# Optimization experiments

Measured on AMD Instinct MI355X. Metric: run time of the kernel, lower is better.

The kernel has to match this reference:

```python
import jax, jax.numpy as jnp
import numpy as np

S, B, I, H = 2048, 4096, 2, 6  # seq, batch, input_size, hidden_size


def setup_inputs() -> dict:
    key = jax.random.key(0)
    ks = jax.random.split(key, 11)
    init = lambda k, sh: jax.random.normal(k, sh, dtype=jnp.float32) * 0.1
    return {
        "x": jax.random.normal(ks[0], (S, B, I), dtype=jnp.float32),
        # layer-0 LSTM params (PyTorch gate order: i, f, g, o)
        "Wih0": init(ks[1], (4 * H, I)),
        "Whh0": init(ks[2], (4 * H, H)),
        "bih0": init(ks[3], (4 * H,)),
        "bhh0": init(ks[4], (4 * H,)),
        # layer-1 LSTM params
        "Wih1": init(ks[5], (4 * H, H)),
        "Whh1": init(ks[6], (4 * H, H)),
        "bih1": init(ks[7], (4 * H,)),
        "bhh1": init(ks[8], (4 * H,)),
        # final Linear(6, 1)
        "W2": init(ks[9], (1, H)),
        "b2": init(ks[10], (1,)),
    }


def _lstm_layer(x, Wih, Whh, bih, bhh):
    # x: (S, B, in_dim) -> hidden outputs (S, B, H)
    Bn = x.shape[1]
    Hn = Whh.shape[1]
    b = bih + bhh
    # precompute input projections for all timesteps at once (memory-bound GEMM)
    xg = jnp.einsum("sbi,gi->sbg", x, Wih) + b  # (S, B, 4H)

    def step(carry, xt_g):
        h, c = carry
        g = xt_g + h @ Whh.T  # (B, 4H)
        i, f, gg, o = jnp.split(g, 4, axis=-1)
        i = jax.nn.sigmoid(i)
        f = jax.nn.sigmoid(f)
        gg = jnp.tanh(gg)
        o = jax.nn.sigmoid(o)
        c = f * c + i * gg
        h = o * jnp.tanh(c)
        return (h, c), h

    h0 = jnp.zeros((Bn, Hn), dtype=x.dtype)
    c0 = jnp.zeros((Bn, Hn), dtype=x.dtype)
    _, hs = jax.lax.scan(step, (h0, c0), xg)
    return hs  # (S, B, H)


def reference(x, Wih0, Whh0, bih0, bhh0, Wih1, Whh1, bih1, bhh1, W2, b2):
    h1 = _lstm_layer(x, Wih0, Whh0, bih0, bhh0)   # (S, B, H)
    h2 = _lstm_layer(h1, Wih1, Whh1, bih1, bhh1)  # (S, B, H); dropout disabled (eval)
    flat = h2.reshape(-1, H)                       # (S*B, H)
    out = flat @ W2.T + b2                         # (S*B, 1) — original discards final view
    return out
```

## Files before the change

### kernel.cpp

```cpp
#include <hip/hip_runtime.h>

#define SEQ   2048
#define BATCH 4096
#define HID   6
#define BLK   256

typedef float v2f __attribute__((ext_vector_type(2)));
typedef unsigned u2 __attribute__((ext_vector_type(2)));

__device__ __forceinline__ float fexp2(float a) {
#if __has_builtin(__builtin_amdgcn_exp2f)
  return __builtin_amdgcn_exp2f(a);
#else
  float r; asm("v_exp_f32 %0, %1" : "=v"(r) : "v"(a)); return r;
#endif
}
__device__ __forceinline__ float frcp(float a) {
#if __has_builtin(__builtin_amdgcn_rcpf)
  return __builtin_amdgcn_rcpf(a);
#else
  float r; asm("v_rcp_f32 %0, %1" : "=v"(r) : "v"(a)); return r;
#endif
}

template <int OFF>
__device__ __forceinline__ float swzf(float v) {
  int r = __builtin_amdgcn_ds_swizzle(__builtin_bit_cast(int, v), OFF);
  return __builtin_bit_cast(float, r);
}
#define BC0 0x18
#define BC1 0x38
#define BC2 0x58
#define BC3 0x78
#define BC4 0x98
#define BC5 0xB8

__device__ __forceinline__ float xhalf(float v, bool hi) {
#if __has_builtin(__builtin_amdgcn_permlane32_swap)
  u2 r = __builtin_amdgcn_permlane32_swap(__builtin_bit_cast(unsigned, v),
                                          __builtin_bit_cast(unsigned, v), false, false);
  return __builtin_bit_cast(float, hi ? r.x : r.y);
#else
  unsigned d = __builtin_bit_cast(unsigned, v), s = d;
  asm volatile("v_permlane32_swap_b32 %0, %1" : "+v"(d), "+v"(s));
  return __builtin_bit_cast(float, hi ? d : s);
#endif
}

__global__ __launch_bounds__(BLK, 1) void lstm2_kernel(
    const float* __restrict__ x,
    const float* __restrict__ Wih0, const float* __restrict__ Whh0,
    const float* __restrict__ bih0, const float* __restrict__ bhh0,
    const float* __restrict__ Wih1, const float* __restrict__ Whh1,
    const float* __restrict__ bih1, const float* __restrict__ bhh1,
    const float* __restrict__ W2,   const float* __restrict__ b2,
    float* __restrict__ out)
{
  __shared__ float obuf[64][16];

  const int tid = threadIdx.x;
  const int wib = tid >> 6;
  const int l6  = tid & 63;
  const bool hi = l6 >= 32;
  const int j   = l6 & 31;
  const int el  = j >> 3;
  const int u   = j & 7;
  const int uu  = (u < HID) ? u : (HID - 1);
  const int b   = blockIdx.x * 16 + wib * 4 + el;

  v2f WA[4][3], WB[4][3];
  float BS[4];
#pragma unroll
  for (int q = 0; q < 4; ++q) {
    const int rq = q * HID + uu;
    const float Kq = (q == 2) ? -2.8853900817779268f : -1.4426950408889634f;
    if (!hi) {
      WA[q][0] = v2f{Kq * Wih0[rq * 2 + 0], Kq * Wih0[rq * 2 + 1]};
      WA[q][1] = v2f{0.f, 0.f};
      WA[q][2] = v2f{0.f, 0.f};
#pragma unroll
      for (int k = 0; k < 3; ++k)
        WB[q][k] = v2f{Kq * Whh0[rq * HID + 2 * k], Kq * Whh0[rq * HID + 2 * k + 1]};
      BS[q] = Kq * (bih0[rq] + bhh0[rq]);
    } else {
#pragma unroll
      for (int k = 0; k < 3; ++k) {
        WA[q][k] = v2f{Kq * Wih1[rq * HID + 2 * k], Kq * Wih1[rq * HID + 2 * k + 1]};
        WB[q][k] = v2f{Kq * Whh1[rq * HID + 2 * k], Kq * Whh1[rq * HID + 2 * k + 1]};
      }
      BS[q] = Kq * (bih1[rq] + bhh1[rq]);
    }
  }
  const v2f w2p0 = v2f{W2[0], W2[1]}, w2p1 = v2f{W2[2], W2[3]}, w2p2 = v2f{W2[4], W2[5]};
  const float bout = b2[0];
  const float KT = 2.8853900817779268f;

  float h = 0.f, c = 0.f;

  auto gath = [&](float hv, v2f (&g)[3]) {
    g[0] = v2f{swzf<BC0>(hv), swzf<BC1>(hv)};
    g[1] = v2f{swzf<BC2>(hv), swzf<BC3>(hv)};
    g[2] = v2f{swzf<BC4>(hv), swzf<BC5>(hv)};
  };

  auto step = [&](v2f xc, float& ov) {
    v2f g2[3]; gath(h, g2);
    float hs = xhalf(h, hi);
    v2f g1[3]; gath(hs, g1);
    v2f v10 = hi ? g1[0] : xc;

    float a[4];
#pragma unroll
    for (int q = 0; q < 4; ++q) {
      v2f acc = v2f{BS[q], 0.f};
      acc = __builtin_elementwise_fma(WA[q][0], v10,   acc);
      acc = __builtin_elementwise_fma(WA[q][1], g1[1], acc);
      acc = __builtin_elementwise_fma(WA[q][2], g1[2], acc);
      acc = __builtin_elementwise_fma(WB[q][0], g2[0], acc);
      acc = __builtin_elementwise_fma(WB[q][1], g2[1], acc);
      acc = __builtin_elementwise_fma(WB[q][2], g2[2], acc);
      a[q] = acc.x + acc.y;
    }
    v2f ao = __builtin_elementwise_fma(w2p0, g2[0],
             __builtin_elementwise_fma(w2p1, g2[1],
             __builtin_elementwise_fma(w2p2, g2[2], v2f{bout, 0.f})));
    ov = ao.x + ao.y;

    float i_ = frcp(1.f + fexp2(a[0]));
    float f_ = frcp(1.f + fexp2(a[1]));
    float g_ = fmaf(2.f, frcp(1.f + fexp2(a[2])), -1.f);
    float o_ = frcp(1.f + fexp2(a[3]));
    c = fmaf(f_, c, i_ * g_);
    float th = fmaf(-2.f, frcp(1.f + fexp2(c * KT)), 1.f);
    h = o_ * th;
  };

  auto flush = [&](int rbase) {
    const int r = tid >> 2, jj = (tid & 3) * 4;
    float4 vv = *(const float4*)&obuf[r][jj];
    *(float4*)&out[(size_t)(rbase + r) * BATCH + blockIdx.x * 16 + jj] = vv;
  };

  const v2f* x2 = (const v2f*)x;
  v2f xc  = x2[(size_t)0 * BATCH + b];
  v2f xn1 = x2[(size_t)1 * BATCH + b];
  v2f xn2 = x2[(size_t)2 * BATCH + b];
  v2f xn3 = x2[(size_t)3 * BATCH + b];

  {
    float ov;
    step(xc, ov);
    if (hi) { h = 0.f; c = 0.f; }
    v2f xf = x2[(size_t)4 * BATCH + b];
    xc = xn1; xn1 = xn2; xn2 = xn3; xn3 = xf;
  }

#pragma unroll 1
  for (int t = 1; t < SEQ; ++t) {
    int tf = t + 4; tf = (tf < SEQ) ? tf : (SEQ - 1);
    v2f xf = x2[(size_t)tf * BATCH + b];

    float ov;
    step(xc, ov);

    if (t >= 2) {
      const int r = t - 2;
      if (hi && u == 0) obuf[r & 63][wib * 4 + el] = ov;
      if ((r & 63) == 63) {
        __syncthreads();
        flush(r - 63);
        __syncthreads();
      }
    }
    xc = xn1; xn1 = xn2; xn2 = xn3; xn3 = xf;
  }

  {
    float ov;
    step(xc, ov);
    if (hi && u == 0) obuf[62][wib * 4 + el] = ov;
    v2f g2[3]; gath(h, g2);
    v2f ao = __builtin_elementwise_fma(w2p0, g2[0],
             __builtin_elementwise_fma(w2p1, g2[1],
             __builtin_elementwise_fma(w2p2, g2[2], v2f{bout, 0.f})));
    if (hi && u == 0) obuf[63][wib * 4 + el] = ao.x + ao.y;
    __syncthreads();
    flush(SEQ - 64);
  }
}

extern "C" void kernel_launch(void* const* d_in, const int* in_sizes, int n_in,
                              void* d_out, int out_size, void* d_ws, size_t ws_size,
                              hipStream_t stream) {
  const float* x    = (const float*)d_in[0];
  const float* Wih0 = (const float*)d_in[1];
  const float* Whh0 = (const float*)d_in[2];
  const float* bih0 = (const float*)d_in[3];
  const float* bhh0 = (const float*)d_in[4];
  const float* Wih1 = (const float*)d_in[5];
  const float* Whh1 = (const float*)d_in[6];
  const float* bih1 = (const float*)d_in[7];
  const float* bhh1 = (const float*)d_in[8];
  const float* W2   = (const float*)d_in[9];
  const float* b2   = (const float*)d_in[10];
  float* out = (float*)d_out;

  dim3 grid(BATCH / 16);
  dim3 block(BLK);
  hipLaunchKernelGGL(lstm2_kernel, grid, block, 0, stream,
                     x, Wih0, Whh0, bih0, bhh0, Wih1, Whh1, bih1, bhh1, W2, b2, out);
}
```

Measured before the change: 621.0 us.

## Replace ds_swizzle broadcasts with DPP xor-permutation gather and permuted weights

Swaps the six ds_swizzle broadcasts per gather for DPP quad and row permutations (xor patterns). Each lane then receives hidden values in a lane-dependent order, so the weight matrices are pre-permuted per lane by u^k with zero padding for the lanes beyond HID. The aim is to drop the LDS-path swizzle latency from the serial recurrence and keep cross-lane movement in VALU DPP. The cost is an extra v2f FMA per gate and split accumulators to shorten the dependency chain.

```diff
diff --git a/kernel.cpp b/kernel.cpp
--- a/kernel.cpp
+++ b/kernel.cpp
@@ -23,17 +23,11 @@
 #endif
 }
 
-template <int OFF>
-__device__ __forceinline__ float swzf(float v) {
-  int r = __builtin_amdgcn_ds_swizzle(__builtin_bit_cast(int, v), OFF);
+template <int CTRL>
+__device__ __forceinline__ float dppf(float v) {
+  int r = __builtin_amdgcn_update_dpp(0, __builtin_bit_cast(int, v), CTRL, 0xF, 0xF, true);
   return __builtin_bit_cast(float, r);
 }
-#define BC0 0x18
-#define BC1 0x38
-#define BC2 0x58
-#define BC3 0x78
-#define BC4 0x98
-#define BC5 0xB8
 
 __device__ __forceinline__ float xhalf(float v, bool hi) {
 #if __has_builtin(__builtin_amdgcn_permlane32_swap)
@@ -68,62 +62,78 @@
   const int uu  = (u < HID) ? u : (HID - 1);
   const int b   = blockIdx.x * 16 + wib * 4 + el;
 
-  v2f WA[4][3], WB[4][3];
+  v2f WA[4][4], WB[4][4], w2r[4];
   float BS[4];
 #pragma unroll
   for (int q = 0; q < 4; ++q) {
     const int rq = q * HID + uu;
     const float Kq = (q == 2) ? -2.8853900817779268f : -1.4426950408889634f;
-    if (!hi) {
-      WA[q][0] = v2f{Kq * Wih0[rq * 2 + 0], Kq * Wih0[rq * 2 + 1]};
-      WA[q][1] = v2f{0.f, 0.f};
-      WA[q][2] = v2f{0.f, 0.f};
-#pragma unroll
-      for (int k = 0; k < 3; ++k)
-        WB[q][k] = v2f{Kq * Whh0[rq * HID + 2 * k], Kq * Whh0[rq * HID + 2 * k + 1]};
-      BS[q] = Kq * (bih0[rq] + bhh0[rq]);
-    } else {
-#pragma unroll
-      for (int k = 0; k < 3; ++k) {
-        WA[q][k] = v2f{Kq * Wih1[rq * HID + 2 * k], Kq * Wih1[rq * HID + 2 * k + 1]};
-        WB[q][k] = v2f{Kq * Whh1[rq * HID + 2 * k], Kq * Whh1[rq * HID + 2 * k + 1]};
+#pragma unroll
+    for (int k = 0; k < 4; ++k) {
+      const int k0 = u ^ (2 * k), k1 = u ^ (2 * k + 1);
+      const bool ok0 = (k0 < HID), ok1 = (k1 < HID);
+      if (!hi) {
+        WA[q][k] = v2f{0.f, 0.f};
+        WB[q][k] = v2f{ok0 ? Kq * Whh0[rq * HID + k0] : 0.f,
+                       ok1 ? Kq * Whh0[rq * HID + k1] : 0.f};
+      } else {
+        WA[q][k] = v2f{ok0 ? Kq * Wih1[rq * HID + k0] : 0.f,
+                       ok1 ? Kq * Wih1[rq * HID + k1] : 0.f};
+        WB[q][k] = v2f{ok0 ? Kq * Whh1[rq * HID + k0] : 0.f,
+                       ok1 ? Kq * Whh1[rq * HID + k1] : 0.f};
       }
-      BS[q] = Kq * (bih1[rq] + bhh1[rq]);
     }
-  }
-  const v2f w2p0 = v2f{W2[0], W2[1]}, w2p1 = v2f{W2[2], W2[3]}, w2p2 = v2f{W2[4], W2[5]};
+    if (!hi) WA[q][0] = v2f{Kq * Wih0[rq * 2 + 0], Kq * Wih0[rq * 2 + 1]};
+    BS[q] = Kq * ((!hi ? bih0[rq] : bih1[rq]) + (!hi ? bhh0[rq] : bhh1[rq]));
+  }
+#pragma unroll
+  for (int k = 0; k < 4; ++k) {
+    const int k0 = u ^ (2 * k), k1 = u ^ (2 * k + 1);
+    w2r[k] = v2f{(k0 < HID) ? W2[k0] : 0.f, (k1 < HID) ? W2[k1] : 0.f};
+  }
   const float bout = b2[0];
   const float KT = 2.8853900817779268f;
 
   float h = 0.f, c = 0.f;
 
-  auto gath = [&](float hv, v2f (&g)[3]) {
-    g[0] = v2f{swzf<BC0>(hv), swzf<BC1>(hv)};
-    g[1] = v2f{swzf<BC2>(hv), swzf<BC3>(hv)};
-    g[2] = v2f{swzf<BC4>(hv), swzf<BC5>(hv)};
+  auto gath = [&](float hv, v2f (&g)[4]) {
+    float t1 = dppf<0xB1>(hv);
+    float t2 = dppf<0x4E>(hv);
+    float t3 = dppf<0x4E>(t1);
+    float m  = dppf<0x141>(hv);
+    float m1 = dppf<0xB1>(m);
+    float m2 = dppf<0x4E>(m);
+    float m3 = dppf<0x4E>(m1);
+    g[0] = v2f{hv, t1};
+    g[1] = v2f{t2, t3};
+    g[2] = v2f{m3, m2};
+    g[3] = v2f{m1, m};
   };
 
   auto step = [&](v2f xc, float& ov) {
-    v2f g2[3]; gath(h, g2);
+    v2f g2[4]; gath(h, g2);
     float hs = xhalf(h, hi);
-    v2f g1[3]; gath(hs, g1);
+    v2f g1[4]; gath(hs, g1);
     v2f v10 = hi ? g1[0] : xc;
 
     float a[4];
 #pragma unroll
     for (int q = 0; q < 4; ++q) {
-      v2f acc = v2f{BS[q], 0.f};
-      acc = __builtin_elementwise_fma(WA[q][0], v10,   acc);
-      acc = __builtin_elementwise_fma(WA[q][1], g1[1], acc);
-      acc = __builtin_elementwise_fma(WA[q][2], g1[2], acc);
-      acc = __builtin_elementwise_fma(WB[q][0], g2[0], acc);
-      acc = __builtin_elementwise_fma(WB[q][1], g2[1], acc);
-      acc = __builtin_elementwise_fma(WB[q][2], g2[2], acc);
+      v2f accA = __builtin_elementwise_fma(WA[q][0], v10, v2f{BS[q], 0.f});
+      accA = __builtin_elementwise_fma(WA[q][1], g1[1], accA);
+      accA = __builtin_elementwise_fma(WA[q][2], g1[2], accA);
+      accA = __builtin_elementwise_fma(WA[q][3], g1[3], accA);
+      v2f accB = WB[q][0] * g2[0];
+      accB = __builtin_elementwise_fma(WB[q][1], g2[1], accB);
+      accB = __builtin_elementwise_fma(WB[q][2], g2[2], accB);
+      accB = __builtin_elementwise_fma(WB[q][3], g2[3], accB);
+      v2f acc = accA + accB;
       a[q] = acc.x + acc.y;
     }
-    v2f ao = __builtin_elementwise_fma(w2p0, g2[0],
-             __builtin_elementwise_fma(w2p1, g2[1],
-             __builtin_elementwise_fma(w2p2, g2[2], v2f{bout, 0.f})));
+    v2f ao = __builtin_elementwise_fma(w2r[0], g2[0],
+             __builtin_elementwise_fma(w2r[1], g2[1],
+             __builtin_elementwise_fma(w2r[2], g2[2],
+             __builtin_elementwise_fma(w2r[3], g2[3], v2f{bout, 0.f}))));
     ov = ao.x + ao.y;
 
     float i_ = frcp(1.f + fexp2(a[0]));
@@ -179,10 +189,11 @@
     float ov;
     step(xc, ov);
     if (hi && u == 0) obuf[62][wib * 4 + el] = ov;
-    v2f g2[3]; gath(h, g2);
-    v2f ao = __builtin_elementwise_fma(w2p0, g2[0],
-             __builtin_elementwise_fma(w2p1, g2[1],
-             __builtin_elementwise_fma(w2p2, g2[2], v2f{bout, 0.f})));
+    v2f g2[4]; gath(h, g2);
+    v2f ao = __builtin_elementwise_fma(w2r[0], g2[0],
+             __builtin_elementwise_fma(w2r[1], g2[1],
+             __builtin_elementwise_fma(w2r[2], g2[2],
+             __builtin_elementwise_fma(w2r[3], g2[3], v2f{bout, 0.f}))));
     if (hi && u == 0) obuf[63][wib * 4 + el] = ao.x + ao.y;
     __syncthreads();
     flush(SEQ - 64);
```

New measurement: 651.4 us. 4.9% more time.

## Split LSTM gate computation across lane pairs to double parallelism per batch element

Applied to the files above, without the earlier changes.

Each batch element now uses 32 lanes instead of 16, so each lane computes only two of the four gates, and the partner gates are exchanged with a DPP row shift. The grid doubles to 8 batch elements per block, and launch bounds allow two blocks per CU. The intent is to shorten the serial per-timestep dependency chain (fewer FMAs and transcendentals per lane) and raise occupancy. The cost is twice as many lanes doing the gather swizzles and an extra cross-lane exchange each step.

```diff
diff --git a/kernel.cpp b/kernel.cpp
--- a/kernel.cpp
+++ b/kernel.cpp
@@ -23,6 +23,12 @@
 #endif
 }
 
+template <int CTRL>
+__device__ __forceinline__ float dppf(float v) {
+  int r = __builtin_amdgcn_update_dpp(0, __builtin_bit_cast(int, v), CTRL, 0xF, 0xF, true);
+  return __builtin_bit_cast(float, r);
+}
+
 template <int OFF>
 __device__ __forceinline__ float swzf(float v) {
   int r = __builtin_amdgcn_ds_swizzle(__builtin_bit_cast(int, v), OFF);
@@ -35,19 +41,19 @@
 #define BC4 0x98
 #define BC5 0xB8
 
-__device__ __forceinline__ float xhalf(float v, bool hi) {
-#if __has_builtin(__builtin_amdgcn_permlane32_swap)
-  u2 r = __builtin_amdgcn_permlane32_swap(__builtin_bit_cast(unsigned, v),
+__device__ __forceinline__ float xor16f(float v, bool hi) {
+#if __has_builtin(__builtin_amdgcn_permlane16_swap)
+  u2 r = __builtin_amdgcn_permlane16_swap(__builtin_bit_cast(unsigned, v),
                                           __builtin_bit_cast(unsigned, v), false, false);
   return __builtin_bit_cast(float, hi ? r.x : r.y);
 #else
   unsigned d = __builtin_bit_cast(unsigned, v), s = d;
-  asm volatile("v_permlane32_swap_b32 %0, %1" : "+v"(d), "+v"(s));
+  asm volatile("v_permlane16_swap_b32 %0, %1" : "+v"(d), "+v"(s));
   return __builtin_bit_cast(float, hi ? d : s);
 #endif
 }
 
-__global__ __launch_bounds__(BLK, 1) void lstm2_kernel(
+__global__ __launch_bounds__(BLK, 2) void lstm2_kernel(
     const float* __restrict__ x,
     const float* __restrict__ Wih0, const float* __restrict__ Whh0,
     const float* __restrict__ bih0, const float* __restrict__ bhh0,
@@ -56,44 +62,54 @@
     const float* __restrict__ W2,   const float* __restrict__ b2,
     float* __restrict__ out)
 {
-  __shared__ float obuf[64][16];
+  __shared__ float obuf[64][8];
 
   const int tid = threadIdx.x;
   const int wib = tid >> 6;
   const int l6  = tid & 63;
-  const bool hi = l6 >= 32;
-  const int j   = l6 & 31;
-  const int el  = j >> 3;
-  const int u   = j & 7;
+  const int el  = l6 >> 5;
+  const int r5  = l6 & 31;
+  const bool hiL = (r5 & 16) != 0;
+  const int p   = (r5 >> 3) & 1;
+  const int u   = r5 & 7;
   const int uu  = (u < HID) ? u : (HID - 1);
-  const int b   = blockIdx.x * 16 + wib * 4 + el;
-
-  v2f WA[4][3], WB[4][3];
-  float BS[4];
+  const int b   = blockIdx.x * 8 + wib * 2 + el;
+
+  const int r0 = p ? (2 * HID + uu) : uu;
+  const int r1 = p ? (3 * HID + uu) : (HID + uu);
+  const float A  = p ? 2.f : 1.f;
+  const float Bc = p ? -1.f : 0.f;
+  const float K0 = p ? -2.8853900817779268f : -1.4426950408889634f;
+  const float K1 = -1.4426950408889634f;
+  const float KT =  2.8853900817779268f;
+
+  v2f WA0[3], WA1[3], WB0[3], WB1[3];
+  float BS0, BS1;
+  if (!hiL) {
+    WA0[0] = v2f{K0 * Wih0[r0 * 2 + 0], K0 * Wih0[r0 * 2 + 1]};
+    WA1[0] = v2f{K1 * Wih0[r1 * 2 + 0], K1 * Wih0[r1 * 2 + 1]};
+    WA0[1] = v2f{0.f, 0.f}; WA0[2] = v2f{0.f, 0.f};
+    WA1[1] = v2f{0.f, 0.f}; WA1[2] = v2f{0.f, 0.f};
 #pragma unroll
-  for (int q = 0; q < 4; ++q) {
-    const int rq = q * HID + uu;
-    const float Kq = (q == 2) ? -2.8853900817779268f : -1.4426950408889634f;
-    if (!hi) {
-      WA[q][0] = v2f{Kq * Wih0[rq * 2 + 0], Kq * Wih0[rq * 2 + 1]};
-      WA[q][1] = v2f{0.f, 0.f};
-      WA[q][2] = v2f{0.f, 0.f};
+    for (int k = 0; k < 3; ++k) {
+      WB0[k] = v2f{K0 * Whh0[r0 * HID + 2 * k], K0 * Whh0[r0 * HID + 2 * k + 1]};
+      WB1[k] = v2f{K1 * Whh0[r1 * HID + 2 * k], K1 * Whh0[r1 * HID + 2 * k + 1]};
+    }
+    BS0 = K0 * (bih0[r0] + bhh0[r0]);
+    BS1 = K1 * (bih0[r1] + bhh0[r1]);
+  } else {
 #pragma unroll
-      for (int k = 0; k < 3; ++k)
-        WB[q][k] = v2f{Kq * Whh0[rq * HID + 2 * k], Kq * Whh0[rq * HID + 2 * k + 1]};
-      BS[q] = Kq * (bih0[rq] + bhh0[rq]);
-    } else {
-#pragma unroll
-      for (int k = 0; k < 3; ++k) {
-        WA[q][k] = v2f{Kq * Wih1[rq * HID + 2 * k], Kq * Wih1[rq * HID + 2 * k + 1]};
-        WB[q][k] = v2f{Kq * Whh1[rq * HID + 2 * k], Kq * Whh1[rq * HID + 2 * k + 1]};
-      }
-      BS[q] = Kq * (bih1[rq] + bhh1[rq]);
+    for (int k = 0; k < 3; ++k) {
+      WA0[k] = v2f{K0 * Wih1[r0 * HID + 2 * k], K0 * Wih1[r0 * HID + 2 * k + 1]};
+      WA1[k] = v2f{K1 * Wih1[r1 * HID + 2 * k], K1 * Wih1[r1 * HID + 2 * k + 1]};
+      WB0[k] = v2f{K0 * Whh1[r0 * HID + 2 * k], K0 * Whh1[r0 * HID + 2 * k + 1]};
+      WB1[k] = v2f{K1 * Whh1[r1 * HID + 2 * k], K1 * Whh1[r1 * HID + 2 * k + 1]};
     }
+    BS0 = K0 * (bih1[r0] + bhh1[r0]);
+    BS1 = K1 * (bih1[r1] + bhh1[r1]);
   }
   const v2f w2p0 = v2f{W2[0], W2[1]}, w2p1 = v2f{W2[2], W2[3]}, w2p2 = v2f{W2[4], W2[5]};
   const float bout = b2[0];
-  const float KT = 2.8853900817779268f;
 
   float h = 0.f, c = 0.f;
 
@@ -105,40 +121,47 @@
 
   auto step = [&](v2f xc, float& ov) {
     v2f g2[3]; gath(h, g2);
-    float hs = xhalf(h, hi);
+    float hs = xor16f(h, hiL);
     v2f g1[3]; gath(hs, g1);
-    v2f v10 = hi ? g1[0] : xc;
-
-    float a[4];
-#pragma unroll
-    for (int q = 0; q < 4; ++q) {
-      v2f acc = v2f{BS[q], 0.f};
-      acc = __builtin_elementwise_fma(WA[q][0], v10,   acc);
-      acc = __builtin_elementwise_fma(WA[q][1], g1[1], acc);
-      acc = __builtin_elementwise_fma(WA[q][2], g1[2], acc);
-      acc = __builtin_elementwise_fma(WB[q][0], g2[0], acc);
-      acc = __builtin_elementwise_fma(WB[q][1], g2[1], acc);
-      acc = __builtin_elementwise_fma(WB[q][2], g2[2], acc);
-      a[q] = acc.x + acc.y;
-    }
+    v2f v10 = hiL ? g1[0] : xc;
+
+    v2f a0v = __builtin_elementwise_fma(WA0[0], v10, v2f{BS0, 0.f});
+    a0v = __builtin_elementwise_fma(WA0[1], g1[1], a0v);
+    a0v = __builtin_elementwise_fma(WA0[2], g1[2], a0v);
+    a0v = __builtin_elementwise_fma(WB0[0], g2[0], a0v);
+    a0v = __builtin_elementwise_fma(WB0[1], g2[1], a0v);
+    a0v = __builtin_elementwise_fma(WB0[2], g2[2], a0v);
+    float a0 = a0v.x + a0v.y;
+
+    v2f a1v = __builtin_elementwise_fma(WA1[0], v10, v2f{BS1, 0.f});
+    a1v = __builtin_elementwise_fma(WA1[1], g1[1], a1v);
+    a1v = __builtin_elementwise_fma(WA1[2], g1[2], a1v);
+    a1v = __builtin_elementwise_fma(WB1[0], g2[0], a1v);
+    a1v = __builtin_elementwise_fma(WB1[1], g2[1], a1v);
+    a1v = __builtin_elementwise_fma(WB1[2], g2[2], a1v);
+    float a1 = a1v.x + a1v.y;
+
     v2f ao = __builtin_elementwise_fma(w2p0, g2[0],
              __builtin_elementwise_fma(w2p1, g2[1],
              __builtin_elementwise_fma(w2p2, g2[2], v2f{bout, 0.f})));
     ov = ao.x + ao.y;
 
-    float i_ = frcp(1.f + fexp2(a[0]));
-    float f_ = frcp(1.f + fexp2(a[1]));
-    float g_ = fmaf(2.f, frcp(1.f + fexp2(a[2])), -1.f);
-    float o_ = frcp(1.f + fexp2(a[3]));
-    c = fmaf(f_, c, i_ * g_);
+    float g0  = fmaf(A, frcp(1.f + fexp2(a0)), Bc);
+    float g1v = frcp(1.f + fexp2(a1));
+    float xg0 = dppf<0x128>(g0);
+    float xg1 = dppf<0x128>(g1v);
+    float m = g0 * xg0;
+    float f = p ? xg1 : g1v;
+    float o = p ? g1v : xg1;
+    c = fmaf(f, c, m);
     float th = fmaf(-2.f, frcp(1.f + fexp2(c * KT)), 1.f);
-    h = o_ * th;
+    h = o * th;
   };
 
   auto flush = [&](int rbase) {
-    const int r = tid >> 2, jj = (tid & 3) * 4;
-    float4 vv = *(const float4*)&obuf[r][jj];
-    *(float4*)&out[(size_t)(rbase + r) * BATCH + blockIdx.x * 16 + jj] = vv;
+    const int r = tid >> 2, jj = (tid & 3) * 2;
+    float2 vv = *(const float2*)&obuf[r][jj];
+    *(float2*)&out[(size_t)(rbase + r) * BATCH + blockIdx.x * 8 + jj] = vv;
   };
 
   const v2f* x2 = (const v2f*)x;
@@ -150,7 +173,7 @@
   {
     float ov;
     step(xc, ov);
-    if (hi) { h = 0.f; c = 0.f; }
+    if (hiL) { h = 0.f; c = 0.f; }
     v2f xf = x2[(size_t)4 * BATCH + b];
     xc = xn1; xn1 = xn2; xn2 = xn3; xn3 = xf;
   }
@@ -165,7 +188,7 @@
 
     if (t >= 2) {
       const int r = t - 2;
-      if (hi && u == 0) obuf[r & 63][wib * 4 + el] = ov;
+      if (hiL && p == 0 && u == 0) obuf[r & 63][wib * 2 + el] = ov;
       if ((r & 63) == 63) {
         __syncthreads();
         flush(r - 63);
@@ -178,12 +201,12 @@
   {
     float ov;
     step(xc, ov);
-    if (hi && u == 0) obuf[62][wib * 4 + el] = ov;
+    if (hiL && p == 0 && u == 0) obuf[62][wib * 2 + el] = ov;
     v2f g2[3]; gath(h, g2);
     v2f ao = __builtin_elementwise_fma(w2p0, g2[0],
              __builtin_elementwise_fma(w2p1, g2[1],
              __builtin_elementwise_fma(w2p2, g2[2], v2f{bout, 0.f})));
-    if (hi && u == 0) obuf[63][wib * 4 + el] = ao.x + ao.y;
+    if (hiL && p == 0 && u == 0) obuf[63][wib * 2 + el] = ao.x + ao.y;
     __syncthreads();
     flush(SEQ - 64);
   }
@@ -205,7 +228,7 @@
   const float* b2   = (const float*)d_in[10];
   float* out = (float*)d_out;
 
-  dim3 grid(BATCH / 16);
+  dim3 grid(BATCH / 8);
   dim3 block(BLK);
   hipLaunchKernelGGL(lstm2_kernel, grid, block, 0, stream,
                      x, Wih0, Whh0, bih0, bhh0, Wih1, Whh1, bih1, bhh1, W2, b2, out);
```

Measured after the change: 669.0 us. +7.7%, slower.

## Stage x in double-buffered LDS chunks and shorten the recurrent dependency chain

Applied to the files above, without the earlier changes.

Replaces the per-step global loads of x (software-pipelined four steps ahead) with coalesced 64-timestep chunk loads into a double-buffered shared-memory tile, refilled during the existing flush barriers. The gather path now runs permlane32_swap on the already-swizzled values instead of swizzling the swapped h again, and each gate dot product is split into two independent FMA chains. The aim is to cut global-load latency and length from the serial per-step critical path. In exchange it adds 16 KB of LDS, per-step LDS reads, and six permlane swaps in place of one swap plus six swizzles.

```diff
diff --git a/kernel.cpp b/kernel.cpp
--- a/kernel.cpp
+++ b/kernel.cpp
@@ -57,6 +57,7 @@
     float* __restrict__ out)
 {
   __shared__ float obuf[64][16];
+  __shared__ float xbuf[2][64][32];
 
   const int tid = threadIdx.x;
   const int wib = tid >> 6;
@@ -66,7 +67,8 @@
   const int el  = j >> 3;
   const int u   = j & 7;
   const int uu  = (u < HID) ? u : (HID - 1);
-  const int b   = blockIdx.x * 16 + wib * 4 + el;
+  const int elb = wib * 4 + el;
+  const int b   = blockIdx.x * 16 + elb;
 
   v2f WA[4][3], WB[4][3];
   float BS[4];
@@ -105,20 +107,22 @@
 
   auto step = [&](v2f xc, float& ov) {
     v2f g2[3]; gath(h, g2);
-    float hs = xhalf(h, hi);
-    v2f g1[3]; gath(hs, g1);
+    v2f g1[3];
+    g1[0] = v2f{xhalf(g2[0].x, hi), xhalf(g2[0].y, hi)};
+    g1[1] = v2f{xhalf(g2[1].x, hi), xhalf(g2[1].y, hi)};
+    g1[2] = v2f{xhalf(g2[2].x, hi), xhalf(g2[2].y, hi)};
     v2f v10 = hi ? g1[0] : xc;
 
     float a[4];
 #pragma unroll
     for (int q = 0; q < 4; ++q) {
-      v2f acc = v2f{BS[q], 0.f};
-      acc = __builtin_elementwise_fma(WA[q][0], v10,   acc);
-      acc = __builtin_elementwise_fma(WA[q][1], g1[1], acc);
-      acc = __builtin_elementwise_fma(WA[q][2], g1[2], acc);
-      acc = __builtin_elementwise_fma(WB[q][0], g2[0], acc);
-      acc = __builtin_elementwise_fma(WB[q][1], g2[1], acc);
-      acc = __builtin_elementwise_fma(WB[q][2], g2[2], acc);
+      v2f accA = __builtin_elementwise_fma(WA[q][0], v10, v2f{BS[q], 0.f});
+      accA = __builtin_elementwise_fma(WA[q][1], g1[1], accA);
+      accA = __builtin_elementwise_fma(WA[q][2], g1[2], accA);
+      v2f accB = WB[q][0] * g2[0];
+      accB = __builtin_elementwise_fma(WB[q][1], g2[1], accB);
+      accB = __builtin_elementwise_fma(WB[q][2], g2[2], accB);
+      v2f acc = accA + accB;
       a[q] = acc.x + acc.y;
     }
     v2f ao = __builtin_elementwise_fma(w2p0, g2[0],
@@ -141,49 +145,71 @@
     *(float4*)&out[(size_t)(rbase + r) * BATCH + blockIdx.x * 16 + jj] = vv;
   };
 
-  const v2f* x2 = (const v2f*)x;
-  v2f xc  = x2[(size_t)0 * BATCH + b];
-  v2f xn1 = x2[(size_t)1 * BATCH + b];
-  v2f xn2 = x2[(size_t)2 * BATCH + b];
-  v2f xn3 = x2[(size_t)3 * BATCH + b];
+  {
+    const int row = tid >> 2, jo = (tid & 3) * 8;
+    const float* s0 = x + (size_t)row * (BATCH * 2) + blockIdx.x * 32 + jo;
+    const float* s1 = s0 + (size_t)64 * (BATCH * 2);
+    float4 a0 = *(const float4*)s0, a1 = *(const float4*)(s0 + 4);
+    float4 b0 = *(const float4*)s1, b1 = *(const float4*)(s1 + 4);
+    *(float4*)&xbuf[0][row][jo]     = a0;
+    *(float4*)&xbuf[0][row][jo + 4] = a1;
+    *(float4*)&xbuf[1][row][jo]     = b0;
+    *(float4*)&xbuf[1][row][jo + 4] = b1;
+    __syncthreads();
+  }
+
+  v2f xr = *(const v2f*)&xbuf[0][0][elb * 2];
 
   {
     float ov;
-    step(xc, ov);
+    step(xr, ov);
     if (hi) { h = 0.f; c = 0.f; }
-    v2f xf = x2[(size_t)4 * BATCH + b];
-    xc = xn1; xn1 = xn2; xn2 = xn3; xn3 = xf;
+    xr = *(const v2f*)&xbuf[0][1][elb * 2];
   }
 
 #pragma unroll 1
   for (int t = 1; t < SEQ; ++t) {
-    int tf = t + 4; tf = (tf < SEQ) ? tf : (SEQ - 1);
-    v2f xf = x2[(size_t)tf * BATCH + b];
+    const int tn = (t + 1 < SEQ) ? t + 1 : SEQ - 1;
+    v2f xnew = *(const v2f*)&xbuf[(tn >> 6) & 1][tn & 63][elb * 2];
 
     float ov;
-    step(xc, ov);
+    step(xr, ov);
 
     if (t >= 2) {
       const int r = t - 2;
-      if (hi && u == 0) obuf[r & 63][wib * 4 + el] = ov;
+      if (hi && u == 0) obuf[r & 63][elb] = ov;
       if ((r & 63) == 63) {
+        const int ck = (t >> 6) + 1;
+        const bool doR = (ck * 64 < SEQ);
+        const int row = tid >> 2, jo = (tid & 3) * 8;
+        float4 a0, a1;
+        if (doR) {
+          const float* src = x + ((size_t)(ck * 64) + row) * (BATCH * 2)
+                               + blockIdx.x * 32 + jo;
+          a0 = *(const float4*)src;
+          a1 = *(const float4*)(src + 4);
+        }
         __syncthreads();
         flush(r - 63);
+        if (doR) {
+          *(float4*)&xbuf[ck & 1][row][jo]     = a0;
+          *(float4*)&xbuf[ck & 1][row][jo + 4] = a1;
+        }
         __syncthreads();
       }
     }
-    xc = xn1; xn1 = xn2; xn2 = xn3; xn3 = xf;
+    xr = xnew;
   }
 
   {
     float ov;
-    step(xc, ov);
-    if (hi && u == 0) obuf[62][wib * 4 + el] = ov;
+    step(xr, ov);
+    if (hi && u == 0) obuf[62][elb] = ov;
     v2f g2[3]; gath(h, g2);
     v2f ao = __builtin_elementwise_fma(w2p0, g2[0],
              __builtin_elementwise_fma(w2p1, g2[1],
              __builtin_elementwise_fma(w2p2, g2[2], v2f{bout, 0.f})));
-    if (hi && u == 0) obuf[63][wib * 4 + el] = ao.x + ao.y;
+    if (hi && u == 0) obuf[63][elb] = ao.x + ao.y;
     __syncthreads();
     flush(SEQ - 64);
   }
```

After: 660.9 us. 1.06x slower.
